# Optimization experiments

Hardware: AMD Instinct MI355X
Metric: run time of the kernel (lower is better)

## Reference

```python
import jax, jax.numpy as jnp
import numpy as np

# config constants (from init_kwargs config['masking'])
MASK_RATIO = 0.15
SPAN_MIN = 5
SPAN_MAX = 20


def _generate_batch_masks(key, batch_size, seq_len):
    """Span-based random masking, exact-count adjusted. [B, S] bool."""
    target_masked = int(seq_len * MASK_RATIO)              # static
    avg_span = (SPAN_MIN + SPAN_MAX) / 2.0
    n_spans = max(1, int(target_masked / avg_span * 2))    # estimated_spans
    k_len, k_start, k_noise = jax.random.split(key, 3)

    span_lengths = jax.random.randint(k_len, (batch_size, n_spans), SPAN_MIN, SPAN_MAX + 1)
    starts = jax.random.randint(k_start, (batch_size, n_spans), 0, max(1, seq_len - SPAN_MIN))
    ends = jnp.minimum(starts + span_lengths, seq_len)

    # Span coverage via +1/-1 scatter + cumsum (equivalent to the per-span
    # boolean scatter loop in the torch code, fully on-device).
    b_idx = jnp.arange(batch_size)[:, None]
    delta = jnp.zeros((batch_size, seq_len + 1), jnp.int32)
    delta = delta.at[b_idx, starts].add(1).at[b_idx, ends].add(-1)
    coverage = jnp.cumsum(delta[:, :seq_len], axis=1) > 0   # [B, S] bool

    # Exact-count adjustment: equivalent to randomly removing excess masked
    # positions / randomly adding unmasked positions until count == target.
    # Masked positions get score in (1,2), unmasked in (0,1); top-k = keep a
    # random masked subset, fill remainder with random unmasked positions.
    noise = jax.random.uniform(k_noise, (batch_size, seq_len))
    score = coverage.astype(jnp.float32) + noise
    _, top_idx = jax.lax.top_k(score, target_masked)        # [B, target]
    masks = jnp.zeros((batch_size, seq_len), bool).at[b_idx, top_idx].set(True)
    return masks


def setup_inputs() -> dict:
    key = jax.random.key(0)
    k1, k2 = jax.random.split(key)
    features = jax.random.normal(k1, (128, 16384, 6), dtype=jnp.float32)
    mask_token = jax.random.normal(k2, (6,), dtype=jnp.float32) * 0.02
    return {"features": features, "mask_token": mask_token}


def reference(features, mask_token):
    B, S, F = features.shape
    key = jax.random.key(1234)  # plays the role of the module's torch.Generator seed
    masks = _generate_batch_masks(key, B, S)
    # _apply_valid_mask_vectorized: only mask non-NaN positions (channel 0)
    valid = ~jnp.isnan(features[:, :, 0])
    masks = masks & valid
    # apply_mask_to_features: replace masked positions with mask_token
    masked_features = jnp.where(masks[:, :, None], mask_token[None, None, :], features)
    return masked_features
```

## Files before the change

### kernel.cpp

```cpp
#include <hip/hip_runtime.h>
#include <stdint.h>

constexpr int NB = 128;
constexpr int SEQ = 16384;
constexpr int NSPANS = 393;
constexpr uint32_t TGT = 2457u;
constexpr int ROWF = SEQ * 6;
constexpr int ROWF4 = ROWF / 4;
constexpr int HALF4 = ROWF4 / 2;

typedef float f32x4 __attribute__((ext_vector_type(4)));

struct Keys {
  uint32_t klo0, klo1;
  uint32_t khi_s0, khi_s1;
  uint32_t klo_s0, klo_s1;
  uint32_t kn0, kn1;
};

__host__ __device__ inline void tf2x32(uint32_t k0, uint32_t k1,
                                       uint32_t x0, uint32_t x1,
                                       uint32_t& o0, uint32_t& o1) {
  uint32_t ks[3] = {k0, k1, k0 ^ k1 ^ 0x1BD11BDAu};
  uint32_t a = x0 + ks[0], b = x1 + ks[1];
  const uint32_t rot[2][4] = {{13u,15u,26u,6u},{17u,29u,16u,24u}};
#pragma unroll
  for (int i = 0; i < 5; ++i) {
    const uint32_t* r = rot[i & 1];
#pragma unroll
    for (int j = 0; j < 4; ++j) {
      a += b;
      b = (b << r[j]) | (b >> (32u - r[j]));
      b ^= a;
    }
    a += ks[(i + 1) % 3];
    b += ks[(i + 2) % 3] + (uint32_t)(i + 1);
  }
  o0 = a; o1 = b;
}

__device__ inline uint32_t rbits(uint32_t k0, uint32_t k1, uint32_t j) {
  uint32_t o0, o1;
  tf2x32(k0, k1, 0u, j, o0, o1);
  return o0 ^ o1;
}

__global__ __launch_bounds__(1024)
void rowpair_kernel(const float* __restrict__ feat, const float* __restrict__ tok,
                    float* __restrict__ out, Keys K) {
  __shared__ uint32_t hist[4096];
  __shared__ uint32_t cov[SEQ / 32];
  __shared__ uint32_t fm[SEQ / 32];
  __shared__ uint32_t wsum[16], ssum[16];
  __shared__ int tielist[256];
  __shared__ uint32_t sH, sA, sT, sN;
  __shared__ int tieCnt;

  const int t = threadIdx.x;
  const int lane = t & 63;
  const int wid = t >> 6;
  const uint32_t bid = blockIdx.x;
  const uint32_t b = bid >> 1;
  const int h = (int)(bid & 1u);

  for (int i = t; i < 4096; i += 1024) hist[i] = 0u;
  if (t < SEQ / 32) cov[t] = 0u;
  if (t == 0) tieCnt = 0;
  __syncthreads();

  if (t < NSPANS) {
    uint32_t j = b * (uint32_t)NSPANS + (uint32_t)t;
    uint32_t lenb = rbits(K.klo0, K.klo1, j);
    uint32_t len = 5u + (lenb & 15u);
    uint32_t hb = rbits(K.khi_s0, K.khi_s1, j);
    uint32_t lb = rbits(K.klo_s0, K.klo_s1, j);
    const uint32_t span = 16379u;
    uint32_t start = ((hb % span) * 400u + (lb % span)) % span;
    uint32_t end = start + len; if (end > (uint32_t)SEQ) end = SEQ;
    uint32_t w0 = start >> 5, w1 = (end - 1u) >> 5;
    for (uint32_t w = w0; w <= w1; ++w) {
      uint32_t bs = (w == w0) ? (start & 31u) : 0u;
      uint32_t be = (w == w1) ? ((end - 1u) & 31u) : 31u;
      uint32_t n = be - bs + 1u;
      uint32_t m = (n >= 32u) ? 0xFFFFFFFFu : (((1u << n) - 1u) << bs);
      atomicOr(&cov[w], m);
    }
  }
  __syncthreads();

  const uint32_t jb = b << 14;
  uint32_t sr[16];
#pragma unroll
  for (int i = 0; i < 16; ++i) {
    int s = (i << 10) + t;
    uint32_t bits = rbits(K.kn0, K.kn1, jb + (uint32_t)s);
    uint32_t si = (bits >> 9) + (((cov[s >> 5] >> (s & 31)) & 1u) << 23);
    sr[i] = si;
    atomicAdd(&hist[si >> 12], 1u);
  }
  __syncthreads();

  {
    uint32_t mysum = 0;
#pragma unroll
    for (int i = 0; i < 4; ++i) mysum += hist[t * 4 + i];
    uint32_t v = mysum;
#pragma unroll
    for (int off = 1; off < 64; off <<= 1) {
      uint32_t n = __shfl_down(v, off, 64);
      if (lane + off < 64) v += n;
    }
    if (lane == 0) wsum[wid] = v;
    __syncthreads();
    if (t < 16) {
      uint32_t w = wsum[t];
#pragma unroll
      for (int off = 1; off < 16; off <<= 1) {
        uint32_t n = __shfl_down(w, off, 64);
        if (t + off < 16) w += n;
      }
      ssum[t] = w;
    }
    __syncthreads();
    uint32_t mine = v + (ssum[wid] - wsum[wid]);
    uint32_t above = mine - mysum;
    if (above < TGT && TGT <= mine) {
      uint32_t run = above;
      for (int hb = t * 4 + 3; hb >= t * 4; --hb) {
        uint32_t c = hist[hb];
        if (run + c >= TGT) { sH = (uint32_t)hb; sA = run; break; }
        run += c;
      }
    }
  }
  __syncthreads();
  uint32_t H = sH;
  uint32_t targetB = TGT - sA;

  for (int i = t; i < 4096; i += 1024) hist[i] = 0u;
  __syncthreads();

#pragma unroll
  for (int i = 0; i < 16; ++i) {
    uint32_t si = sr[i];
    if ((si >> 12) == H) atomicAdd(&hist[si & 4095u], 1u);
  }
  __syncthreads();
  {
    uint32_t mysum = 0;
#pragma unroll
    for (int i = 0; i < 4; ++i) mysum += hist[t * 4 + i];
    uint32_t v = mysum;
#pragma unroll
    for (int off = 1; off < 64; off <<= 1) {
      uint32_t n = __shfl_down(v, off, 64);
      if (lane + off < 64) v += n;
    }
    if (lane == 0) wsum[wid] = v;
    __syncthreads();
    if (t < 16) {
      uint32_t w = wsum[t];
#pragma unroll
      for (int off = 1; off < 16; off <<= 1) {
        uint32_t n = __shfl_down(w, off, 64);
        if (t + off < 16) w += n;
      }
      ssum[t] = w;
    }
    __syncthreads();
    uint32_t mine = v + (ssum[wid] - wsum[wid]);
    uint32_t above = mine - mysum;
    if (above < targetB && targetB <= mine) {
      uint32_t run = above;
      for (int lb = t * 4 + 3; lb >= t * 4; --lb) {
        uint32_t c = hist[lb];
        if (run + c >= targetB) {
          sT = (H << 12) | (uint32_t)lb;
          sN = targetB - run;
          break;
        }
        run += c;
      }
    }
  }
  __syncthreads();
  uint32_t T = sT, need = sN;

#pragma unroll
  for (int i = 0; i < 16; ++i) {
    int s = (i << 10) + t;
    uint32_t si = sr[i];
    unsigned long long bal = __ballot(si > T);
    if (si == T) {
      int idx = atomicAdd(&tieCnt, 1);
      if (idx < 256) tielist[idx] = s;
    }
    if (lane == 0)       fm[s >> 5] = (uint32_t)bal;
    else if (lane == 32) fm[s >> 5] = (uint32_t)(bal >> 32);
  }
  __syncthreads();
  int tc = tieCnt < 256 ? tieCnt : 256;
  if (t < tc) {
    int s = tielist[t];
    uint32_t rank = 0;
    for (int j = 0; j < tc; ++j) rank += (tielist[j] < s) ? 1u : 0u;
    if (rank < need) atomicOr(&fm[s >> 5], 1u << (s & 31));
  }
  __syncthreads();

  {
    const float t0 = tok[0], t1 = tok[1], t2 = tok[2];
    const float t3 = tok[3], t4 = tok[4], t5 = tok[5];
    const size_t rowBase4 = (size_t)b * ROWF4 + (size_t)h * HALF4;
    const float* rowf = feat + (size_t)b * ROWF;
    const f32x4* rf4 = (const f32x4*)feat + rowBase4;
    f32x4* ro4 = (f32x4*)out + rowBase4;
    const int qbase = h * HALF4;

#pragma unroll
    for (int batch = 0; batch < 3; ++batch) {
      f32x4 v0, v1, v2, v3;
      const int q0 = t + (batch * 4) * 1024;
      v0 = rf4[q0];
      v1 = rf4[q0 + 1024];
      v2 = rf4[q0 + 2048];
      v3 = rf4[q0 + 3072];

      f32x4 vv[4] = {v0, v1, v2, v3};
#pragma unroll
      for (int j = 0; j < 4; ++j) {
        const int qrow = qbase + q0 + j * 1024;
        const int e = qrow * 4;
        const int p0 = e / 6;
        const int c0 = e - p0 * 6;
        const int p1 = (p0 + 1 < SEQ) ? p0 + 1 : SEQ - 1;
        const uint32_t w0 = fm[p0 >> 5];
        const uint32_t w1 = fm[p1 >> 5];
        bool m0 = (w0 >> (p0 & 31)) & 1u;
        bool m1 = (w1 >> (p1 & 31)) & 1u;
        if (m0) {
          float c0v = rowf[p0 * 6];
          m0 = !(c0v != c0v);
        }
        if (m1) {
          float c1v = rowf[p1 * 6];
          m1 = !(c1v != c1v);
        }
        const bool is0 = (c0 == 0), is2 = (c0 == 2);
        const float a0 = is0 ? t0 : (is2 ? t2 : t4);
        const float a1 = is0 ? t1 : (is2 ? t3 : t5);
        const float a2 = is0 ? t2 : (is2 ? t4 : t0);
        const float a3 = is0 ? t3 : (is2 ? t5 : t1);
        const bool u01 = m0;
        const bool u23 = (!is0 && !is2) ? m1 : m0;
        f32x4 v = vv[j];
        v.x = u01 ? a0 : v.x;
        v.y = u01 ? a1 : v.y;
        v.z = u23 ? a2 : v.z;
        v.w = u23 ? a3 : v.w;
        vv[j] = v;
      }
      __builtin_nontemporal_store(vv[0], &ro4[q0]);
      __builtin_nontemporal_store(vv[1], &ro4[q0 + 1024]);
      __builtin_nontemporal_store(vv[2], &ro4[q0 + 2048]);
      __builtin_nontemporal_store(vv[3], &ro4[q0 + 3072]);
    }
  }
}

extern "C" void kernel_launch(void* const* d_in, const int* in_sizes, int n_in,
                              void* d_out, int out_size, void* d_ws, size_t ws_size,
                              hipStream_t stream) {
  const float* feat = (const float*)d_in[0];
  const float* tok = (const float*)d_in[1];
  float* out = (float*)d_out;

  uint32_t klen0, klen1, kst0, kst1, kn0, kn1;
  tf2x32(0u, 1234u, 0u, 0u, klen0, klen1);
  tf2x32(0u, 1234u, 0u, 1u, kst0, kst1);
  tf2x32(0u, 1234u, 0u, 2u, kn0, kn1);
  uint32_t lh0, lh1, ll0, ll1;
  tf2x32(klen0, klen1, 0u, 0u, lh0, lh1);
  tf2x32(klen0, klen1, 0u, 1u, ll0, ll1);
  (void)lh0; (void)lh1;
  uint32_t sh0, sh1, sl0, sl1;
  tf2x32(kst0, kst1, 0u, 0u, sh0, sh1);
  tf2x32(kst0, kst1, 0u, 1u, sl0, sl1);
  Keys K{ ll0, ll1, sh0, sh1, sl0, sl1, kn0, kn1 };

  hipLaunchKernelGGL(rowpair_kernel, dim3(2 * NB), dim3(1024), 0, stream,
                     feat, tok, out, K);
}
```

Before: 115.1 us.

## Prefetch feature loads before mask selection and fold NaN check into mask build

Each block now issues eight of its twelve 16-byte feature loads per thread at kernel start, so the HBM reads overlap with the RNG, histogram and top-k selection phases instead of starting only after them. The NaN validity check on channel 0 moves into the final-mask ballot and the tie pass, restricted to positions in this block's half, so the output loop no longer makes dependent scalar global loads. Output stores switch from nontemporal to ordinary stores. Holding 32 extra VGPRs per thread through the selection phase raises register pressure at 1024 threads per block, which can cause spills.

```diff
diff --git a/kernel.cpp b/kernel.cpp
--- a/kernel.cpp
+++ b/kernel.cpp
@@ -43,6 +43,29 @@
   uint32_t o0, o1;
   tf2x32(k0, k1, 0u, j, o0, o1);
   return o0 ^ o1;
+}
+
+__device__ inline f32x4 tok_select(f32x4 v, int qrow, const uint32_t* fm,
+                                   float t0, float t1, float t2,
+                                   float t3, float t4, float t5) {
+  const int e = qrow * 4;
+  const int p0 = e / 6;
+  const int c0 = e - p0 * 6;
+  const int p1 = (p0 + 1) & (SEQ - 1);
+  const uint32_t m0 = (fm[p0 >> 5] >> (p0 & 31)) & 1u;
+  const uint32_t m1 = (fm[p1 >> 5] >> (p1 & 31)) & 1u;
+  const bool is0 = (c0 == 0), is2 = (c0 == 2);
+  const float a0 = is0 ? t0 : (is2 ? t2 : t4);
+  const float a1 = is0 ? t1 : (is2 ? t3 : t5);
+  const float a2 = is0 ? t2 : (is2 ? t4 : t0);
+  const float a3 = is0 ? t3 : (is2 ? t5 : t1);
+  const bool u01 = m0 != 0u;
+  const bool u23 = (!is0 && !is2) ? (m1 != 0u) : (m0 != 0u);
+  v.x = u01 ? a0 : v.x;
+  v.y = u01 ? a1 : v.y;
+  v.z = u23 ? a2 : v.z;
+  v.w = u23 ? a3 : v.w;
+  return v;
 }
 
 __global__ __launch_bounds__(1024)
@@ -62,6 +85,19 @@
   const uint32_t bid = blockIdx.x;
   const uint32_t b = bid >> 1;
   const int h = (int)(bid & 1u);
+
+  const size_t rowBase4 = (size_t)b * ROWF4 + (size_t)h * HALF4;
+  const f32x4* rf4 = (const f32x4*)feat + rowBase4;
+  const float* rowf = feat + (size_t)b * ROWF;
+
+  f32x4 s0 = rf4[t];
+  f32x4 s1 = rf4[t + 1024];
+  f32x4 s2 = rf4[t + 2048];
+  f32x4 s3 = rf4[t + 3072];
+  f32x4 s4 = rf4[t + 4096];
+  f32x4 s5 = rf4[t + 5120];
+  f32x4 s6 = rf4[t + 6144];
+  f32x4 s7 = rf4[t + 7168];
 
   for (int i = t; i < 4096; i += 1024) hist[i] = 0u;
   if (t < SEQ / 32) cov[t] = 0u;
@@ -190,7 +226,13 @@
   for (int i = 0; i < 16; ++i) {
     int s = (i << 10) + t;
     uint32_t si = sr[i];
-    unsigned long long bal = __ballot(si > T);
+    bool sel = si > T;
+    const bool ours = (h == 0) ? (i < 8) : (i >= 8);
+    if (ours && sel) {
+      float c0v = rowf[(size_t)s * 6];
+      sel = !(c0v != c0v);
+    }
+    unsigned long long bal = __ballot(sel);
     if (si == T) {
       int idx = atomicAdd(&tieCnt, 1);
       if (idx < 256) tielist[idx] = s;
@@ -204,67 +246,39 @@
     int s = tielist[t];
     uint32_t rank = 0;
     for (int j = 0; j < tc; ++j) rank += (tielist[j] < s) ? 1u : 0u;
-    if (rank < need) atomicOr(&fm[s >> 5], 1u << (s & 31));
+    if (rank < need) {
+      const bool ours = (h == 0) ? (s < SEQ / 2) : (s >= SEQ / 2);
+      if (ours) {
+        float c0v = rowf[(size_t)s * 6];
+        if (!(c0v != c0v)) atomicOr(&fm[s >> 5], 1u << (s & 31));
+      }
+    }
   }
   __syncthreads();
 
   {
     const float t0 = tok[0], t1 = tok[1], t2 = tok[2];
     const float t3 = tok[3], t4 = tok[4], t5 = tok[5];
-    const size_t rowBase4 = (size_t)b * ROWF4 + (size_t)h * HALF4;
-    const float* rowf = feat + (size_t)b * ROWF;
-    const f32x4* rf4 = (const f32x4*)feat + rowBase4;
     f32x4* ro4 = (f32x4*)out + rowBase4;
     const int qbase = h * HALF4;
 
-#pragma unroll
-    for (int batch = 0; batch < 3; ++batch) {
-      f32x4 v0, v1, v2, v3;
-      const int q0 = t + (batch * 4) * 1024;
-      v0 = rf4[q0];
-      v1 = rf4[q0 + 1024];
-      v2 = rf4[q0 + 2048];
-      v3 = rf4[q0 + 3072];
-
-      f32x4 vv[4] = {v0, v1, v2, v3};
-#pragma unroll
-      for (int j = 0; j < 4; ++j) {
-        const int qrow = qbase + q0 + j * 1024;
-        const int e = qrow * 4;
-        const int p0 = e / 6;
-        const int c0 = e - p0 * 6;
-        const int p1 = (p0 + 1 < SEQ) ? p0 + 1 : SEQ - 1;
-        const uint32_t w0 = fm[p0 >> 5];
-        const uint32_t w1 = fm[p1 >> 5];
-        bool m0 = (w0 >> (p0 & 31)) & 1u;
-        bool m1 = (w1 >> (p1 & 31)) & 1u;
-        if (m0) {
-          float c0v = rowf[p0 * 6];
-          m0 = !(c0v != c0v);
-        }
-        if (m1) {
-          float c1v = rowf[p1 * 6];
-          m1 = !(c1v != c1v);
-        }
-        const bool is0 = (c0 == 0), is2 = (c0 == 2);
-        const float a0 = is0 ? t0 : (is2 ? t2 : t4);
-        const float a1 = is0 ? t1 : (is2 ? t3 : t5);
-        const float a2 = is0 ? t2 : (is2 ? t4 : t0);
-        const float a3 = is0 ? t3 : (is2 ? t5 : t1);
-        const bool u01 = m0;
-        const bool u23 = (!is0 && !is2) ? m1 : m0;
-        f32x4 v = vv[j];
-        v.x = u01 ? a0 : v.x;
-        v.y = u01 ? a1 : v.y;
-        v.z = u23 ? a2 : v.z;
-        v.w = u23 ? a3 : v.w;
-        vv[j] = v;
-      }
-      __builtin_nontemporal_store(vv[0], &ro4[q0]);
-      __builtin_nontemporal_store(vv[1], &ro4[q0 + 1024]);
-      __builtin_nontemporal_store(vv[2], &ro4[q0 + 2048]);
-      __builtin_nontemporal_store(vv[3], &ro4[q0 + 3072]);
-    }
+    f32x4 b8  = rf4[t + 8192];
+    f32x4 b9  = rf4[t + 9216];
+    f32x4 b10 = rf4[t + 10240];
+    f32x4 b11 = rf4[t + 11264];
+
+    ro4[t]         = tok_select(s0, qbase + t,         fm, t0, t1, t2, t3, t4, t5);
+    ro4[t + 1024]  = tok_select(s1, qbase + t + 1024,  fm, t0, t1, t2, t3, t4, t5);
+    ro4[t + 2048]  = tok_select(s2, qbase + t + 2048,  fm, t0, t1, t2, t3, t4, t5);
+    ro4[t + 3072]  = tok_select(s3, qbase + t + 3072,  fm, t0, t1, t2, t3, t4, t5);
+    ro4[t + 4096]  = tok_select(s4, qbase + t + 4096,  fm, t0, t1, t2, t3, t4, t5);
+    ro4[t + 5120]  = tok_select(s5, qbase + t + 5120,  fm, t0, t1, t2, t3, t4, t5);
+    ro4[t + 6144]  = tok_select(s6, qbase + t + 6144,  fm, t0, t1, t2, t3, t4, t5);
+    ro4[t + 7168]  = tok_select(s7, qbase + t + 7168,  fm, t0, t1, t2, t3, t4, t5);
+    ro4[t + 8192]  = tok_select(b8,  qbase + t + 8192,  fm, t0, t1, t2, t3, t4, t5);
+    ro4[t + 9216]  = tok_select(b9,  qbase + t + 9216,  fm, t0, t1, t2, t3, t4, t5);
+    ro4[t + 10240] = tok_select(b10, qbase + t + 10240, fm, t0, t1, t2, t3, t4, t5);
+    ro4[t + 11264] = tok_select(b11, qbase + t + 11264, fm, t0, t1, t2, t3, t4, t5);
   }
 }
 
```

After: 118.6 us. +3.0%, slower.

## Copy features first, then scatter mask tokens only at masked positions

Applied to the files above, without the earlier changes.

The kernel now starts with a plain vectorized copy of its half-row from input to output, so the memory traffic is issued before the mask computation. After the mask is built, a sparse pass writes the mask token only at masked, non-NaN positions, replacing the per-element select pass. Most __syncthreads are replaced by an LDS waitcnt plus s_barrier, and launch bounds request higher occupancy so the copy of one block can overlap the compute of others. The masked positions are written twice, and correctness relies on the global write ordering within each thread, which holds because the same thread does not write both; a __syncthreads still separates the copy from the scatter.

```diff
diff --git a/kernel.cpp b/kernel.cpp
--- a/kernel.cpp
+++ b/kernel.cpp
@@ -45,7 +45,12 @@
   return o0 ^ o1;
 }
 
-__global__ __launch_bounds__(1024)
+__device__ inline void bar_lds() {
+  asm volatile("s_waitcnt lgkmcnt(0)" ::: "memory");
+  __builtin_amdgcn_s_barrier();
+}
+
+__global__ __launch_bounds__(1024, 4)
 void rowpair_kernel(const float* __restrict__ feat, const float* __restrict__ tok,
                     float* __restrict__ out, Keys K) {
   __shared__ uint32_t hist[4096];
@@ -63,10 +68,41 @@
   const uint32_t b = bid >> 1;
   const int h = (int)(bid & 1u);
 
+  const size_t rowBase4 = (size_t)b * ROWF4 + (size_t)h * HALF4;
+  const f32x4* rf4 = (const f32x4*)feat + rowBase4;
+  f32x4* ro4 = (f32x4*)out + rowBase4;
+
+  {
+    f32x4 v0 = rf4[t];
+    f32x4 v1 = rf4[t + 1024];
+    f32x4 v2 = rf4[t + 2048];
+    f32x4 v3 = rf4[t + 3072];
+    f32x4 v4 = rf4[t + 4096];
+    f32x4 v5 = rf4[t + 5120];
+    f32x4 v6 = rf4[t + 6144];
+    f32x4 v7 = rf4[t + 7168];
+    ro4[t]        = v0;
+    ro4[t + 1024] = v1;
+    ro4[t + 2048] = v2;
+    ro4[t + 3072] = v3;
+    f32x4 v8  = rf4[t + 8192];
+    f32x4 v9  = rf4[t + 9216];
+    f32x4 v10 = rf4[t + 10240];
+    f32x4 v11 = rf4[t + 11264];
+    ro4[t + 4096] = v4;
+    ro4[t + 5120] = v5;
+    ro4[t + 6144] = v6;
+    ro4[t + 7168] = v7;
+    ro4[t + 8192]  = v8;
+    ro4[t + 9216]  = v9;
+    ro4[t + 10240] = v10;
+    ro4[t + 11264] = v11;
+  }
+
   for (int i = t; i < 4096; i += 1024) hist[i] = 0u;
   if (t < SEQ / 32) cov[t] = 0u;
   if (t == 0) tieCnt = 0;
-  __syncthreads();
+  bar_lds();
 
   if (t < NSPANS) {
     uint32_t j = b * (uint32_t)NSPANS + (uint32_t)t;
@@ -86,7 +122,7 @@
       atomicOr(&cov[w], m);
     }
   }
-  __syncthreads();
+  bar_lds();
 
   const uint32_t jb = b << 14;
   uint32_t sr[16];
@@ -98,7 +134,7 @@
     sr[i] = si;
     atomicAdd(&hist[si >> 12], 1u);
   }
-  __syncthreads();
+  bar_lds();
 
   {
     uint32_t mysum = 0;
@@ -111,7 +147,7 @@
       if (lane + off < 64) v += n;
     }
     if (lane == 0) wsum[wid] = v;
-    __syncthreads();
+    bar_lds();
     if (t < 16) {
       uint32_t w = wsum[t];
 #pragma unroll
@@ -121,7 +157,7 @@
       }
       ssum[t] = w;
     }
-    __syncthreads();
+    bar_lds();
     uint32_t mine = v + (ssum[wid] - wsum[wid]);
     uint32_t above = mine - mysum;
     if (above < TGT && TGT <= mine) {
@@ -133,19 +169,19 @@
       }
     }
   }
-  __syncthreads();
+  bar_lds();
   uint32_t H = sH;
   uint32_t targetB = TGT - sA;
 
   for (int i = t; i < 4096; i += 1024) hist[i] = 0u;
-  __syncthreads();
+  bar_lds();
 
 #pragma unroll
   for (int i = 0; i < 16; ++i) {
     uint32_t si = sr[i];
     if ((si >> 12) == H) atomicAdd(&hist[si & 4095u], 1u);
   }
-  __syncthreads();
+  bar_lds();
   {
     uint32_t mysum = 0;
 #pragma unroll
@@ -157,7 +193,7 @@
       if (lane + off < 64) v += n;
     }
     if (lane == 0) wsum[wid] = v;
-    __syncthreads();
+    bar_lds();
     if (t < 16) {
       uint32_t w = wsum[t];
 #pragma unroll
@@ -167,7 +203,7 @@
       }
       ssum[t] = w;
     }
-    __syncthreads();
+    bar_lds();
     uint32_t mine = v + (ssum[wid] - wsum[wid]);
     uint32_t above = mine - mysum;
     if (above < targetB && targetB <= mine) {
@@ -183,7 +219,7 @@
       }
     }
   }
-  __syncthreads();
+  bar_lds();
   uint32_t T = sT, need = sN;
 
 #pragma unroll
@@ -198,7 +234,7 @@
     if (lane == 0)       fm[s >> 5] = (uint32_t)bal;
     else if (lane == 32) fm[s >> 5] = (uint32_t)(bal >> 32);
   }
-  __syncthreads();
+  bar_lds();
   int tc = tieCnt < 256 ? tieCnt : 256;
   if (t < tc) {
     int s = tielist[t];
@@ -206,64 +242,29 @@
     for (int j = 0; j < tc; ++j) rank += (tielist[j] < s) ? 1u : 0u;
     if (rank < need) atomicOr(&fm[s >> 5], 1u << (s & 31));
   }
+
   __syncthreads();
 
-  {
-    const float t0 = tok[0], t1 = tok[1], t2 = tok[2];
-    const float t3 = tok[3], t4 = tok[4], t5 = tok[5];
-    const size_t rowBase4 = (size_t)b * ROWF4 + (size_t)h * HALF4;
-    const float* rowf = feat + (size_t)b * ROWF;
-    const f32x4* rf4 = (const f32x4*)feat + rowBase4;
-    f32x4* ro4 = (f32x4*)out + rowBase4;
-    const int qbase = h * HALF4;
-
-#pragma unroll
-    for (int batch = 0; batch < 3; ++batch) {
-      f32x4 v0, v1, v2, v3;
-      const int q0 = t + (batch * 4) * 1024;
-      v0 = rf4[q0];
-      v1 = rf4[q0 + 1024];
-      v2 = rf4[q0 + 2048];
-      v3 = rf4[q0 + 3072];
-
-      f32x4 vv[4] = {v0, v1, v2, v3};
-#pragma unroll
-      for (int j = 0; j < 4; ++j) {
-        const int qrow = qbase + q0 + j * 1024;
-        const int e = qrow * 4;
-        const int p0 = e / 6;
-        const int c0 = e - p0 * 6;
-        const int p1 = (p0 + 1 < SEQ) ? p0 + 1 : SEQ - 1;
-        const uint32_t w0 = fm[p0 >> 5];
-        const uint32_t w1 = fm[p1 >> 5];
-        bool m0 = (w0 >> (p0 & 31)) & 1u;
-        bool m1 = (w1 >> (p1 & 31)) & 1u;
-        if (m0) {
-          float c0v = rowf[p0 * 6];
-          m0 = !(c0v != c0v);
+  if (t < 512) {
+    const int wi = h * 256 + (t >> 1);
+    const uint32_t w = fm[wi];
+    const uint32_t hw = (w >> ((t & 1) << 4)) & 0xFFFFu;
+    if (hw) {
+      const float2 t01 = make_float2(tok[0], tok[1]);
+      const float2 t23 = make_float2(tok[2], tok[3]);
+      const float2 t45 = make_float2(tok[4], tok[5]);
+      uint32_t hbits = hw;
+      const size_t basePos = (size_t)b * SEQ + (size_t)wi * 32 + (size_t)((t & 1) << 4);
+      while (hbits) {
+        int bit = __ffs(hbits) - 1;
+        hbits &= hbits - 1u;
+        size_t p = basePos + (size_t)bit;
+        float c0 = feat[p * 6];
+        if (!(c0 != c0)) {
+          float2* o = (float2*)(out + p * 6);
+          o[0] = t01; o[1] = t23; o[2] = t45;
         }
-        if (m1) {
-          float c1v = rowf[p1 * 6];
-          m1 = !(c1v != c1v);
-        }
-        const bool is0 = (c0 == 0), is2 = (c0 == 2);
-        const float a0 = is0 ? t0 : (is2 ? t2 : t4);
-        const float a1 = is0 ? t1 : (is2 ? t3 : t5);
-        const float a2 = is0 ? t2 : (is2 ? t4 : t0);
-        const float a3 = is0 ? t3 : (is2 ? t5 : t1);
-        const bool u01 = m0;
-        const bool u23 = (!is0 && !is2) ? m1 : m0;
-        f32x4 v = vv[j];
-        v.x = u01 ? a0 : v.x;
-        v.y = u01 ? a1 : v.y;
-        v.z = u23 ? a2 : v.z;
-        v.w = u23 ? a3 : v.w;
-        vv[j] = v;
-      }
-      __builtin_nontemporal_store(vv[0], &ro4[q0]);
-      __builtin_nontemporal_store(vv[1], &ro4[q0 + 1024]);
-      __builtin_nontemporal_store(vv[2], &ro4[q0 + 2048]);
-      __builtin_nontemporal_store(vv[3], &ro4[q0 + 3072]);
+      }
     }
   }
 }
```

New measurement: 114.6 us. About the same (-0.4%).

## Split into bulk copy kernel plus sparse masked-position fixup kernel

Applied to the files above, without the earlier changes.

Replaces the fused per-row mask-and-copy with two launches: a plain vectorized copy of all features to the output, then a mask kernel (one block per row) that computes the mask and writes the token only at masked, non-NaN positions. The copy can now run at full streaming bandwidth across many small blocks, and the mask work no longer gates the stream. In exchange the copy drops nontemporal stores, there is an extra launch, the mask kernel's grid is halved to 128 blocks, and the sparse fixup writes are scattered 8-byte stores.

```diff
diff --git a/kernel.cpp b/kernel.cpp
--- a/kernel.cpp
+++ b/kernel.cpp
@@ -7,7 +7,9 @@
 constexpr uint32_t TGT = 2457u;
 constexpr int ROWF = SEQ * 6;
 constexpr int ROWF4 = ROWF / 4;
-constexpr int HALF4 = ROWF4 / 2;
+constexpr int TOT4 = NB * ROWF4;
+constexpr int CP_PT = 4;
+constexpr int CP_BLOCKS = TOT4 / (256 * CP_PT);
 
 typedef float f32x4 __attribute__((ext_vector_type(4)));
 
@@ -45,8 +47,25 @@
   return o0 ^ o1;
 }
 
+
+__global__ __launch_bounds__(256)
+void copy_kernel(const float* __restrict__ feat, float* __restrict__ out) {
+  const size_t base = (size_t)blockIdx.x * (256 * CP_PT) + threadIdx.x;
+  const f32x4* f4 = (const f32x4*)feat;
+  f32x4* o4 = (f32x4*)out;
+  f32x4 v0 = f4[base];
+  f32x4 v1 = f4[base + 256];
+  f32x4 v2 = f4[base + 512];
+  f32x4 v3 = f4[base + 768];
+  __builtin_amdgcn_sched_barrier(0);
+  o4[base]       = v0;
+  o4[base + 256] = v1;
+  o4[base + 512] = v2;
+  o4[base + 768] = v3;
+}
+
 __global__ __launch_bounds__(1024)
-void rowpair_kernel(const float* __restrict__ feat, const float* __restrict__ tok,
+void maskfix_kernel(const float* __restrict__ feat, const float* __restrict__ tok,
                     float* __restrict__ out, Keys K) {
   __shared__ uint32_t hist[4096];
   __shared__ uint32_t cov[SEQ / 32];
@@ -59,9 +78,7 @@
   const int t = threadIdx.x;
   const int lane = t & 63;
   const int wid = t >> 6;
-  const uint32_t bid = blockIdx.x;
-  const uint32_t b = bid >> 1;
-  const int h = (int)(bid & 1u);
+  const uint32_t b = blockIdx.x;
 
   for (int i = t; i < 4096; i += 1024) hist[i] = 0u;
   if (t < SEQ / 32) cov[t] = 0u;
@@ -209,61 +226,24 @@
   __syncthreads();
 
   {
-    const float t0 = tok[0], t1 = tok[1], t2 = tok[2];
-    const float t3 = tok[3], t4 = tok[4], t5 = tok[5];
-    const size_t rowBase4 = (size_t)b * ROWF4 + (size_t)h * HALF4;
-    const float* rowf = feat + (size_t)b * ROWF;
-    const f32x4* rf4 = (const f32x4*)feat + rowBase4;
-    f32x4* ro4 = (f32x4*)out + rowBase4;
-    const int qbase = h * HALF4;
-
-#pragma unroll
-    for (int batch = 0; batch < 3; ++batch) {
-      f32x4 v0, v1, v2, v3;
-      const int q0 = t + (batch * 4) * 1024;
-      v0 = rf4[q0];
-      v1 = rf4[q0 + 1024];
-      v2 = rf4[q0 + 2048];
-      v3 = rf4[q0 + 3072];
-
-      f32x4 vv[4] = {v0, v1, v2, v3};
-#pragma unroll
-      for (int j = 0; j < 4; ++j) {
-        const int qrow = qbase + q0 + j * 1024;
-        const int e = qrow * 4;
-        const int p0 = e / 6;
-        const int c0 = e - p0 * 6;
-        const int p1 = (p0 + 1 < SEQ) ? p0 + 1 : SEQ - 1;
-        const uint32_t w0 = fm[p0 >> 5];
-        const uint32_t w1 = fm[p1 >> 5];
-        bool m0 = (w0 >> (p0 & 31)) & 1u;
-        bool m1 = (w1 >> (p1 & 31)) & 1u;
-        if (m0) {
-          float c0v = rowf[p0 * 6];
-          m0 = !(c0v != c0v);
+    const uint32_t w = fm[t >> 1];
+    uint32_t hw = (w >> ((t & 1) << 4)) & 0xFFFFu;
+    if (hw) {
+      const float2 t01 = make_float2(tok[0], tok[1]);
+      const float2 t23 = make_float2(tok[2], tok[3]);
+      const float2 t45 = make_float2(tok[4], tok[5]);
+      const size_t basePos = (size_t)b * SEQ + (size_t)(t >> 1) * 32
+                           + (size_t)((t & 1) << 4);
+      while (hw) {
+        int bit = __ffs(hw) - 1;
+        hw &= hw - 1u;
+        size_t p = basePos + (size_t)bit;
+        float c0 = feat[p * 6];
+        if (!(c0 != c0)) {
+          float2* o = (float2*)(out + p * 6);
+          o[0] = t01; o[1] = t23; o[2] = t45;
         }
-        if (m1) {
-          float c1v = rowf[p1 * 6];
-          m1 = !(c1v != c1v);
-        }
-        const bool is0 = (c0 == 0), is2 = (c0 == 2);
-        const float a0 = is0 ? t0 : (is2 ? t2 : t4);
-        const float a1 = is0 ? t1 : (is2 ? t3 : t5);
-        const float a2 = is0 ? t2 : (is2 ? t4 : t0);
-        const float a3 = is0 ? t3 : (is2 ? t5 : t1);
-        const bool u01 = m0;
-        const bool u23 = (!is0 && !is2) ? m1 : m0;
-        f32x4 v = vv[j];
-        v.x = u01 ? a0 : v.x;
-        v.y = u01 ? a1 : v.y;
-        v.z = u23 ? a2 : v.z;
-        v.w = u23 ? a3 : v.w;
-        vv[j] = v;
-      }
-      __builtin_nontemporal_store(vv[0], &ro4[q0]);
-      __builtin_nontemporal_store(vv[1], &ro4[q0 + 1024]);
-      __builtin_nontemporal_store(vv[2], &ro4[q0 + 2048]);
-      __builtin_nontemporal_store(vv[3], &ro4[q0 + 3072]);
+      }
     }
   }
 }
@@ -288,6 +268,7 @@
   tf2x32(kst0, kst1, 0u, 1u, sl0, sl1);
   Keys K{ ll0, ll1, sh0, sh1, sl0, sl1, kn0, kn1 };
 
-  hipLaunchKernelGGL(rowpair_kernel, dim3(2 * NB), dim3(1024), 0, stream,
+  hipLaunchKernelGGL(copy_kernel, dim3(CP_BLOCKS), dim3(256), 0, stream, feat, out);
+  hipLaunchKernelGGL(maskfix_kernel, dim3(NB), dim3(1024), 0, stream,
                      feat, tok, out, K);
 }
```

Result: slower. 124.1 us (+7.8%).
